# Kernel tuning notes

Measured on AMD Instinct MI355X. Metric: run time of the kernel, lower is better.

The kernel has to match this reference:

```python
import jax, jax.numpy as jnp
import numpy as np


def _ward_agglomerative(xf: np.ndarray, k: int) -> np.ndarray:
    """Ward-linkage agglomerative clustering (sklearn default), returning
    integer labels in [0, k) for each of the n rows of xf.

    Sequential Lance-Williams merge loop: this IS the algorithm's math and is
    inherently sequential (the reason this module has kernel headroom).
    Per-merge updates are fully vectorized over the n 'other' clusters.
    """
    xf = np.asarray(xf, dtype=np.float64)
    n = xf.shape[0]
    # initial squared-euclidean distances (Ward criterion on singletons)
    sq = np.sum(xf * xf, axis=1)
    d2 = sq[:, None] + sq[None, :] - 2.0 * (xf @ xf.T)
    np.maximum(d2, 0.0, out=d2)
    np.fill_diagonal(d2, np.inf)

    sizes = np.ones(n, dtype=np.float64)
    active = np.ones(n, dtype=bool)
    cluster_of = np.arange(n)  # point -> current representative cluster id
    idxs = np.arange(n)

    for _ in range(n - k):
        flat = np.argmin(d2)  # inactive rows/cols are +inf
        i, j = divmod(flat, n)
        if i > j:
            i, j = j, i
        dij = d2[i, j]
        si, sj = sizes[i], sizes[j]
        m = active.copy()
        m[i] = False
        m[j] = False
        sm = sizes[m]
        # Lance-Williams Ward update on squared distances (vectorized over m)
        new_d = ((si + sm) * d2[i, m] + (sj + sm) * d2[j, m] - sm * dij) / (si + sj + sm)
        d2[i, m] = new_d
        d2[m, i] = new_d
        sizes[i] = si + sj
        active[j] = False
        d2[j, :] = np.inf
        d2[:, j] = np.inf
        d2[i, i] = np.inf
        cluster_of[cluster_of == j] = i

    # relabel surviving cluster ids to 0..k-1 by first occurrence
    _, labels = np.unique(cluster_of, return_inverse=True)
    return labels.astype(np.int32)


def setup_inputs() -> dict:
    key = jax.random.key(0)
    x = jax.random.uniform(key, (4, 512, 96), dtype=jnp.float32)  # [B, N, D]
    return {"x": x, "num_clusters": 100}


def reference(x, num_clusters):
    # Faithful translation of HierarchicalClustering.forward:
    # flatten batch+tokens, Ward agglomerative clustering, one-hot scatter.
    B, N, D = x.shape
    xf = np.asarray(jax.device_get(x)).reshape(B * N, D)
    labels = _ward_agglomerative(xf, int(num_clusters))  # [B*N]
    onehot = jax.nn.one_hot(jnp.asarray(labels), int(num_clusters), dtype=jnp.float32)
    return onehot.reshape(B, N, int(num_clusters))
```

## Files before the change

kernel.cpp:

```cpp
#include <hip/hip_runtime.h>
#include <math.h>

#define NPTS   2048
#define DIM    96
#define PITCH  2048
#define TB     8
#define ROUNDS 48

__device__ double g_cent[DIM * PITCH];
__device__ double g_sz[NPTS];
__device__ double g_nrm[NPTS];
__device__ int    g_act[NPTS];
__device__ int    g_cidx[NPTS];
__device__ double g_nnv[NPTS];
__device__ int    g_nni[NPTS];
__device__ int    g_reci[NPTS];
__device__ int    g_recj[NPTS];
__device__ double g_rech[NPTS];
__device__ int    g_a, g_done, g_mcount;

__global__ void init_kernel(const float* __restrict__ x) {
    int p = blockIdx.x * 256 + threadIdx.x;
    if (p < NPTS) {
        double nr = 0.0;
        for (int d = 0; d < DIM; ++d) {
            double v = (double)x[p * DIM + d];
            g_cent[d * PITCH + p] = v;
            nr += v * v;
        }
        g_nrm[p] = nr; g_sz[p] = 1.0; g_act[p] = 1; g_cidx[p] = p;
        g_nni[p] = -1; g_nnv[p] = (double)INFINITY;
        g_reci[p] = 0; g_recj[p] = 0; g_rech[p] = (double)INFINITY;
    }
    if (p == 0) { g_a = NPTS; g_done = 0; g_mcount = 0; }
}

__global__ void __launch_bounds__(512) nn_pass() {
    if (g_done) return;
    const int a = g_a;
    const int tile0 = blockIdx.x * TB;
    if (tile0 >= a) return;
    const int t = threadIdx.x;

    __shared__ int    sIdx[TB];
    __shared__ double sMu[DIM * TB];
    __shared__ double sNb[TB], sSb[TB];
    __shared__ double sRedV[8 * TB];
    __shared__ int    sRedI[8 * TB];

    if (t < TB) {
        int cm   = tile0 + t;
        int orig = (cm < a) ? g_cidx[cm] : -1;
        sIdx[t] = orig;
        sNb[t]  = (orig >= 0) ? g_nrm[orig] : 0.0;
        sSb[t]  = (orig >= 0) ? g_sz[orig]  : 1.0;
    }
    __syncthreads();
    for (int e = t; e < DIM * TB; e += 512) {
        int col = sIdx[e & 7];
        sMu[e] = (col >= 0) ? g_cent[(e >> 3) * PITCH + col] : 0.0;
    }
    __syncthreads();

    int om[4]; bool vld[4];
#pragma unroll
    for (int q = 0; q < 4; ++q) {
        int m  = t + q * 512;
        vld[q] = (m < a);
        om[q]  = g_cidx[vld[q] ? m : (a - 1)];
    }

    double acc[4][TB];
#pragma unroll
    for (int q = 0; q < 4; ++q)
#pragma unroll
        for (int bi = 0; bi < TB; ++bi) acc[q][bi] = 0.0;

    for (int d = 0; d < DIM; ++d) {
        double mu[TB];
#pragma unroll
        for (int bi = 0; bi < TB; ++bi) mu[bi] = sMu[d * TB + bi];
        double x0 = g_cent[d * PITCH + om[0]];
        double x1 = g_cent[d * PITCH + om[1]];
        double x2 = g_cent[d * PITCH + om[2]];
        double x3 = g_cent[d * PITCH + om[3]];
#pragma unroll
        for (int bi = 0; bi < TB; ++bi) {
            acc[0][bi] += mu[bi] * x0;
            acc[1][bi] += mu[bi] * x1;
            acc[2][bi] += mu[bi] * x2;
            acc[3][bi] += mu[bi] * x3;
        }
    }

    double bv[TB]; int bidx[TB];
#pragma unroll
    for (int bi = 0; bi < TB; ++bi) { bv[bi] = (double)INFINITY; bidx[bi] = 0x7FFFFFFF; }
#pragma unroll
    for (int q = 0; q < 4; ++q) {
        if (!vld[q]) continue;
        int    cm = t + q * 512;
        double sm = g_sz[om[q]], nm = g_nrm[om[q]];
#pragma unroll
        for (int bi = 0; bi < TB; ++bi) {
            double f = (sSb[bi] * sm) / (sSb[bi] + sm);
            double D = (2.0 * f) * ((sNb[bi] + nm) - 2.0 * acc[q][bi]);
            if (cm != tile0 + bi && D < bv[bi]) { bv[bi] = D; bidx[bi] = om[q]; }
        }
    }

    const int lane = t & 63, w = t >> 6;
#pragma unroll
    for (int bi = 0; bi < TB; ++bi) {
        double v = bv[bi]; int ix = bidx[bi];
        for (int off = 1; off < 64; off <<= 1) {
            double ov = __shfl_xor(v, off);
            int    oi = __shfl_xor(ix, off);
            if (ov < v || (ov == v && oi < ix)) { v = ov; ix = oi; }
        }
        if (lane == 0) { sRedV[w * TB + bi] = v; sRedI[w * TB + bi] = ix; }
    }
    __syncthreads();
    if (t < TB && tile0 + t < a) {
        double v = sRedV[t]; int ix = sRedI[t];
        for (int w2 = 1; w2 < 8; ++w2) {
            double ov = sRedV[w2 * TB + t]; int oi = sRedI[w2 * TB + t];
            if (ov < v || (ov == v && oi < ix)) { v = ov; ix = oi; }
        }
        g_nnv[sIdx[t]] = v;
        g_nni[sIdx[t]] = ix;
    }
}

__global__ void __launch_bounds__(1024) merge_pass() {
    if (g_done) return;
    __shared__ int sWave[16];
    const int t = threadIdx.x, lane = t & 63, w = t >> 6;

    for (int b = t; b < NPTS; b += 1024) {
        int j = g_nni[b];
        if (j > b && j < NPTS && g_nni[j] == b) {
            int r = atomicAdd(&g_mcount, 1);
            g_reci[r] = b; g_recj[r] = j; g_rech[r] = g_nnv[b];
            double sb = g_sz[b], sj = g_sz[j], s2 = sb + sj;
            double nr = 0.0;
            for (int d = 0; d < DIM; ++d) {
                double v = (sb * g_cent[d * PITCH + b] + sj * g_cent[d * PITCH + j]) / s2;
                g_cent[d * PITCH + b] = v;
                nr += v * v;
            }
            g_sz[b] = s2; g_nrm[b] = nr;
            g_act[j] = 0; g_nni[j] = -1; g_nnv[j] = (double)INFINITY;
        }
    }
    __syncthreads();

    int e0 = 2 * t, e1 = 2 * t + 1;
    int c0 = g_act[e0], c1 = g_act[e1];
    int sum = c0 + c1;
    int v = sum;
    for (int off = 1; off < 64; off <<= 1) {
        int o = __shfl_up(v, off);
        if (lane >= off) v += o;
    }
    if (lane == 63) sWave[w] = v;
    __syncthreads();
    if (t == 0) {
        int run = 0;
        for (int i = 0; i < 16; ++i) { int x = sWave[i]; sWave[i] = run; run += x; }
    }
    __syncthreads();
    int base = sWave[w] + (v - sum);
    if (c0) g_cidx[base]      = e0;
    if (c1) g_cidx[base + c0] = e1;
    if (t == 1023) {
        int a2 = base + sum;
        g_a = a2;
        g_done = (a2 <= 1) ? 1 : 0;
    }
}

__global__ void __launch_bounds__(1024) finisher(const int* __restrict__ kptr,
                                                 float* __restrict__ out) {
    __shared__ double D0[NPTS];
    __shared__ int    I0[NPTS];
    __shared__ int    I1[NPTS];
    __shared__ int    I2[NPTS];
    __shared__ int    I3[NPTS];
    __shared__ int    I4[NPTS];
    __shared__ int    sNp;

    const int t = threadIdx.x, lane = t & 63, w = t >> 6;
    const int k = *kptr;
    int a = g_a;

    for (int guard = 0; guard < NPTS && a > 1; ++guard) {
        for (int b = w; b < NPTS; b += 16) {
            if (!g_act[b]) { if (lane == 0) { D0[b] = (double)INFINITY; I0[b] = -1; } continue; }
            double sb = g_sz[b], nb = g_nrm[b];
            double bvv = (double)INFINITY; int bii = 0x7FFFFFFF;
            for (int m = lane; m < NPTS; m += 64) {
                if (!g_act[m] || m == b) continue;
                double dot = 0.0;
                for (int d = 0; d < DIM; ++d)
                    dot += g_cent[d * PITCH + b] * g_cent[d * PITCH + m];
                double sm = g_sz[m], nm = g_nrm[m];
                double f = (sb * sm) / (sb + sm);
                double D = (2.0 * f) * ((nb + nm) - 2.0 * dot);
                if (D < bvv || (D == bvv && m < bii)) { bvv = D; bii = m; }
            }
            for (int off = 1; off < 64; off <<= 1) {
                double ov = __shfl_xor(bvv, off);
                int    oi = __shfl_xor(bii, off);
                if (ov < bvv || (ov == bvv && oi < bii)) { bvv = ov; bii = oi; }
            }
            if (lane == 0) { D0[b] = bvv; I0[b] = bii; }
        }
        __syncthreads();
        if (t == 0) sNp = 0;
        __syncthreads();
        for (int b = t; b < NPTS; b += 1024) {
            int j = I0[b];
            if (j > b && j < NPTS && I0[j] == b) {
                int r = atomicAdd(&g_mcount, 1);
                g_reci[r] = b; g_recj[r] = j; g_rech[r] = D0[b];
                double sb = g_sz[b], sj = g_sz[j], s2 = sb + sj;
                double nr = 0.0;
                for (int d = 0; d < DIM; ++d) {
                    double v = (sb * g_cent[d * PITCH + b] + sj * g_cent[d * PITCH + j]) / s2;
                    g_cent[d * PITCH + b] = v; nr += v * v;
                }
                g_sz[b] = s2; g_nrm[b] = nr; g_act[j] = 0;
                atomicAdd(&sNp, 1);
            }
        }
        __syncthreads();
        a -= sNp;
        __syncthreads();
    }

    const int M    = g_mcount;
    const int nsel = NPTS - k;
    __syncthreads();
    for (int e = t; e < NPTS; e += 1024) {
        D0[e] = (e < M) ? g_rech[e] : (double)INFINITY;
        I0[e] = e;
    }
    __syncthreads();
    for (int k2 = 2; k2 <= NPTS; k2 <<= 1) {
        for (int j2 = k2 >> 1; j2 > 0; j2 >>= 1) {
            for (int i = t; i < NPTS; i += 1024) {
                int ixj = i ^ j2;
                if (ixj > i) {
                    bool up = ((i & k2) == 0);
                    double a0 = D0[i], a1 = D0[ixj];
                    if (up ? (a0 > a1) : (a0 < a1)) {
                        D0[i] = a1; D0[ixj] = a0;
                        int ti_ = I0[i]; I0[i] = I0[ixj]; I0[ixj] = ti_;
                    }
                }
            }
            __syncthreads();
        }
    }
    for (int p = t; p < NPTS; p += 1024) I1[p] = p;
    __syncthreads();
    for (int r = t; r < nsel; r += 1024) {
        int rec = I0[r];
        I1[g_recj[rec]] = g_reci[rec];
    }
    __syncthreads();
    int* psrc = I1; int* pdst = I2;
    for (int it2 = 0; it2 < 11; ++it2) {
        for (int p = t; p < NPTS; p += 1024) pdst[p] = psrc[psrc[p]];
        __syncthreads();
        int* tp = psrc; psrc = pdst; pdst = tp;
    }
    for (int p = t; p < NPTS; p += 1024) I3[p] = (psrc[p] == p) ? 1 : 0;
    __syncthreads();
    int* rsrc = I3; int* rdst = I4;
    for (int off = 1; off < NPTS; off <<= 1) {
        for (int p = t; p < NPTS; p += 1024)
            rdst[p] = rsrc[p] + ((p >= off) ? rsrc[p - off] : 0);
        __syncthreads();
        int* tp = rsrc; rsrc = rdst; rdst = tp;
    }
    for (int p = t; p < NPTS; p += 1024) {
        int lbl = rsrc[psrc[p]] - 1;
        out[(size_t)p * k + lbl] = 1.0f;
    }
}

extern "C" void kernel_launch(void* const* d_in, const int* in_sizes, int n_in,
                              void* d_out, int out_size, void* d_ws, size_t ws_size,
                              hipStream_t stream) {
    const float* x    = (const float*)d_in[0];
    const int*   kptr = (const int*)d_in[1];
    float*       out  = (float*)d_out;

    hipMemsetAsync(d_out, 0, (size_t)out_size * sizeof(float), stream);
    init_kernel<<<8, 256, 0, stream>>>(x);
    for (int r = 0; r < ROUNDS; ++r) {
        nn_pass<<<NPTS / TB, 512, 0, stream>>>();
        merge_pass<<<1, 1024, 0, stream>>>();
    }
    finisher<<<1, 1024, 0, stream>>>(kptr, out);
}
```

Before: 3.475 ms.

## Fuse all clustering rounds into one persistent kernel with grid barriers

Replaces the fixed 48 rounds of nn_pass/merge_pass launches plus the separate init, memset and finisher with a single persistent kernel of 192 blocks. The blocks synchronise through an atomic grid barrier and each keeps its own copy of the active-cluster compaction in shared memory. Rounds run adaptively until fewer than 192 clusters remain, and block 0 then finishes alone. Merges are spread across waves, with 64 lanes working on the dimensions in parallel. This removes launch overhead and the wasted fixed rounds and the serial per-thread merge. The risks are grid-barrier deadlock if not all blocks are co-resident, plus high shared-memory use per block that may limit residency.

```diff
diff --git a/kernel.cpp b/kernel.cpp
--- a/kernel.cpp
+++ b/kernel.cpp
@@ -1,291 +1,336 @@
 #include <hip/hip_runtime.h>
 #include <math.h>
 
-#define NPTS   2048
-#define DIM    96
-#define PITCH  2048
-#define TB     8
-#define ROUNDS 48
+#define NPTS  2048
+#define DIM   96
+#define PITCH 2048
+#define TB    8
+#define NBLK  192
+#define NTHR  512
+#define TAIL  192
 
 __device__ double g_cent[DIM * PITCH];
 __device__ double g_sz[NPTS];
 __device__ double g_nrm[NPTS];
 __device__ int    g_act[NPTS];
-__device__ int    g_cidx[NPTS];
 __device__ double g_nnv[NPTS];
 __device__ int    g_nni[NPTS];
 __device__ int    g_reci[NPTS];
 __device__ int    g_recj[NPTS];
 __device__ double g_rech[NPTS];
-__device__ int    g_a, g_done, g_mcount;
-
-__global__ void init_kernel(const float* __restrict__ x) {
-    int p = blockIdx.x * 256 + threadIdx.x;
-    if (p < NPTS) {
+__device__ int    g_mcount;
+__device__ int    g_barcnt = 0;
+__device__ int    g_bargen = 0;
+
+__device__ __forceinline__ void gridbar() {
+    __syncthreads();
+    if (threadIdx.x == 0) {
+        __threadfence();
+        int gen = __hip_atomic_load(&g_bargen, __ATOMIC_RELAXED, __HIP_MEMORY_SCOPE_AGENT);
+        int prev = __hip_atomic_fetch_add(&g_barcnt, 1, __ATOMIC_ACQ_REL, __HIP_MEMORY_SCOPE_AGENT);
+        if (prev == NBLK - 1) {
+            __hip_atomic_store(&g_barcnt, 0, __ATOMIC_RELAXED, __HIP_MEMORY_SCOPE_AGENT);
+            __hip_atomic_store(&g_bargen, gen + 1, __ATOMIC_RELEASE, __HIP_MEMORY_SCOPE_AGENT);
+        } else {
+            while (__hip_atomic_load(&g_bargen, __ATOMIC_ACQUIRE, __HIP_MEMORY_SCOPE_AGENT) == gen)
+                __builtin_amdgcn_s_sleep(2);
+        }
+        __threadfence();
+    }
+    __syncthreads();
+}
+
+__device__ __forceinline__ int block_compact(unsigned short* sCidx, int* sWS) {
+    const int t = threadIdx.x, lane = t & 63, w = t >> 6;
+    int base = t * 4;
+    int c0 = g_act[base], c1 = g_act[base + 1], c2 = g_act[base + 2], c3 = g_act[base + 3];
+    int sum = c0 + c1 + c2 + c3;
+    int v = sum;
+#pragma unroll
+    for (int off = 1; off < 64; off <<= 1) {
+        int o = __shfl_up(v, off);
+        if (lane >= off) v += o;
+    }
+    if (lane == 63) sWS[w] = v;
+    __syncthreads();
+    if (t == 0) {
+        int run = 0;
+#pragma unroll
+        for (int i = 0; i < 8; ++i) { int x = sWS[i]; sWS[i] = run; run += x; }
+        sWS[8] = run;
+    }
+    __syncthreads();
+    int ex = sWS[w] + (v - sum);
+    if (c0) sCidx[ex] = (unsigned short)base;       ex += c0;
+    if (c1) sCidx[ex] = (unsigned short)(base + 1); ex += c1;
+    if (c2) sCidx[ex] = (unsigned short)(base + 2); ex += c2;
+    if (c3) sCidx[ex] = (unsigned short)(base + 3); ex += c3;
+    int a = sWS[8];
+    __syncthreads();
+    return a;
+}
+
+__device__ __forceinline__ void wave_merge(int b, int j, double hgt, int lane) {
+    double sb = g_sz[b], sj = g_sz[j], s2 = sb + sj;
+    int d0 = lane;
+    double v0 = (sb * g_cent[d0 * PITCH + b] + sj * g_cent[d0 * PITCH + j]) / s2;
+    g_cent[d0 * PITCH + b] = v0;
+    double v1 = 0.0;
+    if (lane < DIM - 64) {
+        int d1 = lane + 64;
+        v1 = (sb * g_cent[d1 * PITCH + b] + sj * g_cent[d1 * PITCH + j]) / s2;
+        g_cent[d1 * PITCH + b] = v1;
+    }
+    double pnr = v0 * v0 + v1 * v1;
+#pragma unroll
+    for (int off = 1; off < 64; off <<= 1)
+        pnr += __shfl_xor(pnr, off);
+    if (lane == 0) {
+        g_sz[b] = s2; g_nrm[b] = pnr; g_act[j] = 0;
+        int r = atomicAdd(&g_mcount, 1);
+        g_reci[r] = b; g_recj[r] = j; g_rech[r] = hgt;
+    }
+}
+
+__global__ void __launch_bounds__(NTHR) fused(const float* __restrict__ x,
+                                              const int* __restrict__ kptr,
+                                              float* __restrict__ out, int out_size) {
+    __shared__ unsigned short sCidx[NPTS];
+    __shared__ double sMu[TB * DIM];
+    __shared__ double sNb[TB], sSb[TB];
+    __shared__ int    sIdx[TB];
+    __shared__ double sRedV[64];
+    __shared__ int    sRedI[64];
+    __shared__ int    sPair[128];
+    __shared__ int    sNp;
+    __shared__ int    sWS[16];
+    __shared__ double fD0[NPTS];
+    __shared__ int    fI0[NPTS];
+    __shared__ int    fI1[NPTS];
+    __shared__ int    fI2[NPTS];
+    __shared__ int    fI3[NPTS];
+    __shared__ int    fI4[NPTS];
+
+    const int bid = blockIdx.x, t = threadIdx.x, lane = t & 63, w = t >> 6;
+
+    for (int i = bid * NTHR + t; i < out_size; i += NBLK * NTHR) out[i] = 0.0f;
+    for (int p = bid * NTHR + t; p < NPTS; p += NBLK * NTHR) {
         double nr = 0.0;
         for (int d = 0; d < DIM; ++d) {
             double v = (double)x[p * DIM + d];
             g_cent[d * PITCH + p] = v;
             nr += v * v;
         }
-        g_nrm[p] = nr; g_sz[p] = 1.0; g_act[p] = 1; g_cidx[p] = p;
-        g_nni[p] = -1; g_nnv[p] = (double)INFINITY;
-        g_reci[p] = 0; g_recj[p] = 0; g_rech[p] = (double)INFINITY;
-    }
-    if (p == 0) { g_a = NPTS; g_done = 0; g_mcount = 0; }
-}
-
-__global__ void __launch_bounds__(512) nn_pass() {
-    if (g_done) return;
-    const int a = g_a;
-    const int tile0 = blockIdx.x * TB;
-    if (tile0 >= a) return;
-    const int t = threadIdx.x;
-
-    __shared__ int    sIdx[TB];
-    __shared__ double sMu[DIM * TB];
-    __shared__ double sNb[TB], sSb[TB];
-    __shared__ double sRedV[8 * TB];
-    __shared__ int    sRedI[8 * TB];
-
-    if (t < TB) {
-        int cm   = tile0 + t;
-        int orig = (cm < a) ? g_cidx[cm] : -1;
-        sIdx[t] = orig;
-        sNb[t]  = (orig >= 0) ? g_nrm[orig] : 0.0;
-        sSb[t]  = (orig >= 0) ? g_sz[orig]  : 1.0;
-    }
-    __syncthreads();
-    for (int e = t; e < DIM * TB; e += 512) {
-        int col = sIdx[e & 7];
-        sMu[e] = (col >= 0) ? g_cent[(e >> 3) * PITCH + col] : 0.0;
-    }
-    __syncthreads();
-
-    int om[4]; bool vld[4];
-#pragma unroll
-    for (int q = 0; q < 4; ++q) {
-        int m  = t + q * 512;
-        vld[q] = (m < a);
-        om[q]  = g_cidx[vld[q] ? m : (a - 1)];
-    }
-
-    double acc[4][TB];
-#pragma unroll
-    for (int q = 0; q < 4; ++q)
-#pragma unroll
-        for (int bi = 0; bi < TB; ++bi) acc[q][bi] = 0.0;
-
-    for (int d = 0; d < DIM; ++d) {
-        double mu[TB];
-#pragma unroll
-        for (int bi = 0; bi < TB; ++bi) mu[bi] = sMu[d * TB + bi];
-        double x0 = g_cent[d * PITCH + om[0]];
-        double x1 = g_cent[d * PITCH + om[1]];
-        double x2 = g_cent[d * PITCH + om[2]];
-        double x3 = g_cent[d * PITCH + om[3]];
-#pragma unroll
-        for (int bi = 0; bi < TB; ++bi) {
-            acc[0][bi] += mu[bi] * x0;
-            acc[1][bi] += mu[bi] * x1;
-            acc[2][bi] += mu[bi] * x2;
-            acc[3][bi] += mu[bi] * x3;
-        }
-    }
-
-    double bv[TB]; int bidx[TB];
-#pragma unroll
-    for (int bi = 0; bi < TB; ++bi) { bv[bi] = (double)INFINITY; bidx[bi] = 0x7FFFFFFF; }
-#pragma unroll
-    for (int q = 0; q < 4; ++q) {
-        if (!vld[q]) continue;
-        int    cm = t + q * 512;
-        double sm = g_sz[om[q]], nm = g_nrm[om[q]];
-#pragma unroll
-        for (int bi = 0; bi < TB; ++bi) {
-            double f = (sSb[bi] * sm) / (sSb[bi] + sm);
-            double D = (2.0 * f) * ((sNb[bi] + nm) - 2.0 * acc[q][bi]);
-            if (cm != tile0 + bi && D < bv[bi]) { bv[bi] = D; bidx[bi] = om[q]; }
-        }
-    }
-
-    const int lane = t & 63, w = t >> 6;
-#pragma unroll
-    for (int bi = 0; bi < TB; ++bi) {
-        double v = bv[bi]; int ix = bidx[bi];
-        for (int off = 1; off < 64; off <<= 1) {
-            double ov = __shfl_xor(v, off);
-            int    oi = __shfl_xor(ix, off);
-            if (ov < v || (ov == v && oi < ix)) { v = ov; ix = oi; }
-        }
-        if (lane == 0) { sRedV[w * TB + bi] = v; sRedI[w * TB + bi] = ix; }
-    }
-    __syncthreads();
-    if (t < TB && tile0 + t < a) {
-        double v = sRedV[t]; int ix = sRedI[t];
-        for (int w2 = 1; w2 < 8; ++w2) {
-            double ov = sRedV[w2 * TB + t]; int oi = sRedI[w2 * TB + t];
-            if (ov < v || (ov == v && oi < ix)) { v = ov; ix = oi; }
-        }
-        g_nnv[sIdx[t]] = v;
-        g_nni[sIdx[t]] = ix;
-    }
-}
-
-__global__ void __launch_bounds__(1024) merge_pass() {
-    if (g_done) return;
-    __shared__ int sWave[16];
-    const int t = threadIdx.x, lane = t & 63, w = t >> 6;
-
-    for (int b = t; b < NPTS; b += 1024) {
-        int j = g_nni[b];
-        if (j > b && j < NPTS && g_nni[j] == b) {
-            int r = atomicAdd(&g_mcount, 1);
-            g_reci[r] = b; g_recj[r] = j; g_rech[r] = g_nnv[b];
-            double sb = g_sz[b], sj = g_sz[j], s2 = sb + sj;
-            double nr = 0.0;
+        g_nrm[p] = nr; g_sz[p] = 1.0; g_act[p] = 1;
+    }
+    if (bid == 0 && t == 0) g_mcount = 0;
+    gridbar();
+
+    int a = block_compact(sCidx, sWS);
+
+    while (a > TAIL) {
+        for (int tile0 = bid * TB; tile0 < a; tile0 += NBLK * TB) {
+            __syncthreads();
+            if (t < TB) {
+                int cm = tile0 + t;
+                int orig = (cm < a) ? (int)sCidx[cm] : -1;
+                sIdx[t] = orig;
+                sNb[t] = (orig >= 0) ? g_nrm[orig] : 0.0;
+                sSb[t] = (orig >= 0) ? g_sz[orig] : 1.0;
+            }
+            __syncthreads();
+            for (int e = t; e < DIM * TB; e += NTHR) {
+                int col = sIdx[e & 7];
+                sMu[e] = (col >= 0) ? g_cent[(e >> 3) * PITCH + col] : 0.0;
+            }
+            __syncthreads();
+
+            int om[4]; bool vld[4];
+#pragma unroll
+            for (int q = 0; q < 4; ++q) {
+                int m = t + q * NTHR;
+                vld[q] = (m < a);
+                om[q] = (int)sCidx[vld[q] ? m : (a - 1)];
+            }
+            double acc[4][TB];
+#pragma unroll
+            for (int q = 0; q < 4; ++q)
+#pragma unroll
+                for (int bi = 0; bi < TB; ++bi) acc[q][bi] = 0.0;
+
             for (int d = 0; d < DIM; ++d) {
-                double v = (sb * g_cent[d * PITCH + b] + sj * g_cent[d * PITCH + j]) / s2;
-                g_cent[d * PITCH + b] = v;
-                nr += v * v;
-            }
-            g_sz[b] = s2; g_nrm[b] = nr;
-            g_act[j] = 0; g_nni[j] = -1; g_nnv[j] = (double)INFINITY;
-        }
-    }
-    __syncthreads();
-
-    int e0 = 2 * t, e1 = 2 * t + 1;
-    int c0 = g_act[e0], c1 = g_act[e1];
-    int sum = c0 + c1;
-    int v = sum;
-    for (int off = 1; off < 64; off <<= 1) {
-        int o = __shfl_up(v, off);
-        if (lane >= off) v += o;
-    }
-    if (lane == 63) sWave[w] = v;
-    __syncthreads();
-    if (t == 0) {
-        int run = 0;
-        for (int i = 0; i < 16; ++i) { int x = sWave[i]; sWave[i] = run; run += x; }
-    }
-    __syncthreads();
-    int base = sWave[w] + (v - sum);
-    if (c0) g_cidx[base]      = e0;
-    if (c1) g_cidx[base + c0] = e1;
-    if (t == 1023) {
-        int a2 = base + sum;
-        g_a = a2;
-        g_done = (a2 <= 1) ? 1 : 0;
-    }
-}
-
-__global__ void __launch_bounds__(1024) finisher(const int* __restrict__ kptr,
-                                                 float* __restrict__ out) {
-    __shared__ double D0[NPTS];
-    __shared__ int    I0[NPTS];
-    __shared__ int    I1[NPTS];
-    __shared__ int    I2[NPTS];
-    __shared__ int    I3[NPTS];
-    __shared__ int    I4[NPTS];
-    __shared__ int    sNp;
-
-    const int t = threadIdx.x, lane = t & 63, w = t >> 6;
-    const int k = *kptr;
-    int a = g_a;
-
-    for (int guard = 0; guard < NPTS && a > 1; ++guard) {
-        for (int b = w; b < NPTS; b += 16) {
-            if (!g_act[b]) { if (lane == 0) { D0[b] = (double)INFINITY; I0[b] = -1; } continue; }
+                double mu[TB];
+#pragma unroll
+                for (int bi = 0; bi < TB; ++bi) mu[bi] = sMu[d * TB + bi];
+                double x0 = g_cent[d * PITCH + om[0]];
+                double x1 = g_cent[d * PITCH + om[1]];
+                double x2 = g_cent[d * PITCH + om[2]];
+                double x3 = g_cent[d * PITCH + om[3]];
+#pragma unroll
+                for (int bi = 0; bi < TB; ++bi) {
+                    acc[0][bi] += mu[bi] * x0;
+                    acc[1][bi] += mu[bi] * x1;
+                    acc[2][bi] += mu[bi] * x2;
+                    acc[3][bi] += mu[bi] * x3;
+                }
+            }
+
+            double bv[TB]; int bidx[TB];
+#pragma unroll
+            for (int bi = 0; bi < TB; ++bi) { bv[bi] = (double)INFINITY; bidx[bi] = 0x7FFFFFFF; }
+#pragma unroll
+            for (int q = 0; q < 4; ++q) {
+                if (!vld[q]) continue;
+                int cm = t + q * NTHR;
+                double sm = g_sz[om[q]], nm = g_nrm[om[q]];
+#pragma unroll
+                for (int bi = 0; bi < TB; ++bi) {
+                    double f = (sSb[bi] * sm) / (sSb[bi] + sm);
+                    double D = (2.0 * f) * ((sNb[bi] + nm) - 2.0 * acc[q][bi]);
+                    if (cm != tile0 + bi && D < bv[bi]) { bv[bi] = D; bidx[bi] = om[q]; }
+                }
+            }
+#pragma unroll
+            for (int bi = 0; bi < TB; ++bi) {
+                double v = bv[bi]; int ix = bidx[bi];
+                for (int off = 1; off < 64; off <<= 1) {
+                    double ov = __shfl_xor(v, off);
+                    int    oi = __shfl_xor(ix, off);
+                    if (ov < v || (ov == v && oi < ix)) { v = ov; ix = oi; }
+                }
+                if (lane == 0) { sRedV[w * TB + bi] = v; sRedI[w * TB + bi] = ix; }
+            }
+            __syncthreads();
+            if (t < TB && tile0 + t < a) {
+                double v = sRedV[t]; int ix = sRedI[t];
+                for (int w2 = 1; w2 < 8; ++w2) {
+                    double ov = sRedV[w2 * TB + t]; int oi = sRedI[w2 * TB + t];
+                    if (ov < v || (ov == v && oi < ix)) { v = ov; ix = oi; }
+                }
+                g_nnv[sIdx[t]] = v;
+                g_nni[sIdx[t]] = ix;
+            }
+        }
+        gridbar();
+
+        if (t == 0) sNp = 0;
+        __syncthreads();
+        for (int tile0 = bid * TB; tile0 < a; tile0 += NBLK * TB) {
+            int cm = tile0 + t;
+            if (t < TB && cm < a) {
+                int b = (int)sCidx[cm];
+                int j = g_nni[b];
+                if (j > b && g_nni[j] == b) {
+                    int s = atomicAdd(&sNp, 1);
+                    sPair[s] = (b << 16) | j;
+                }
+            }
+        }
+        __syncthreads();
+        int np = sNp;
+        for (int p = w; p < np; p += 8) {
+            int pk = sPair[p], b = pk >> 16, jj = pk & 0xFFFF;
+            wave_merge(b, jj, g_nnv[b], lane);
+        }
+        gridbar();
+        a = block_compact(sCidx, sWS);
+    }
+
+    if (bid != 0) return;
+
+    while (a > 1) {
+        for (int c = w; c < a; c += 8) {
+            int b = (int)sCidx[c];
             double sb = g_sz[b], nb = g_nrm[b];
-            double bvv = (double)INFINITY; int bii = 0x7FFFFFFF;
-            for (int m = lane; m < NPTS; m += 64) {
-                if (!g_act[m] || m == b) continue;
+            double bv = (double)INFINITY; int bi2 = 0x7FFFFFFF;
+            for (int cm = lane; cm < a; cm += 64) {
+                int m = (int)sCidx[cm];
+                if (m == b) continue;
                 double dot = 0.0;
                 for (int d = 0; d < DIM; ++d)
                     dot += g_cent[d * PITCH + b] * g_cent[d * PITCH + m];
                 double sm = g_sz[m], nm = g_nrm[m];
                 double f = (sb * sm) / (sb + sm);
                 double D = (2.0 * f) * ((nb + nm) - 2.0 * dot);
-                if (D < bvv || (D == bvv && m < bii)) { bvv = D; bii = m; }
-            }
+                if (D < bv || (D == bv && m < bi2)) { bv = D; bi2 = m; }
+            }
+#pragma unroll
             for (int off = 1; off < 64; off <<= 1) {
-                double ov = __shfl_xor(bvv, off);
-                int    oi = __shfl_xor(bii, off);
-                if (ov < bvv || (ov == bvv && oi < bii)) { bvv = ov; bii = oi; }
-            }
-            if (lane == 0) { D0[b] = bvv; I0[b] = bii; }
+                double ov = __shfl_xor(bv, off);
+                int    oi = __shfl_xor(bi2, off);
+                if (ov < bv || (ov == bv && oi < bi2)) { bv = ov; bi2 = oi; }
+            }
+            if (lane == 0) { fD0[b] = bv; fI0[b] = bi2; }
         }
         __syncthreads();
         if (t == 0) sNp = 0;
         __syncthreads();
-        for (int b = t; b < NPTS; b += 1024) {
-            int j = I0[b];
-            if (j > b && j < NPTS && I0[j] == b) {
-                int r = atomicAdd(&g_mcount, 1);
-                g_reci[r] = b; g_recj[r] = j; g_rech[r] = D0[b];
-                double sb = g_sz[b], sj = g_sz[j], s2 = sb + sj;
-                double nr = 0.0;
-                for (int d = 0; d < DIM; ++d) {
-                    double v = (sb * g_cent[d * PITCH + b] + sj * g_cent[d * PITCH + j]) / s2;
-                    g_cent[d * PITCH + b] = v; nr += v * v;
-                }
-                g_sz[b] = s2; g_nrm[b] = nr; g_act[j] = 0;
-                atomicAdd(&sNp, 1);
-            }
-        }
-        __syncthreads();
-        a -= sNp;
-        __syncthreads();
-    }
-
-    const int M    = g_mcount;
+        for (int c = t; c < a; c += NTHR) {
+            int b = (int)sCidx[c];
+            int j = fI0[b];
+            if (j > b && fI0[j] == b) {
+                int s = atomicAdd(&sNp, 1);
+                sPair[s] = (b << 16) | j;
+            }
+        }
+        __syncthreads();
+        int np = sNp;
+        for (int p = w; p < np; p += 8) {
+            int pk = sPair[p], b = pk >> 16, jj = pk & 0xFFFF;
+            wave_merge(b, jj, fD0[b], lane);
+        }
+        __syncthreads();
+        a = block_compact(sCidx, sWS);
+    }
+
+    const int k = *kptr;
+    const int M = g_mcount;
     const int nsel = NPTS - k;
     __syncthreads();
-    for (int e = t; e < NPTS; e += 1024) {
-        D0[e] = (e < M) ? g_rech[e] : (double)INFINITY;
-        I0[e] = e;
+    for (int e = t; e < NPTS; e += NTHR) {
+        fD0[e] = (e < M) ? g_rech[e] : (double)INFINITY;
+        fI0[e] = e;
     }
     __syncthreads();
     for (int k2 = 2; k2 <= NPTS; k2 <<= 1) {
         for (int j2 = k2 >> 1; j2 > 0; j2 >>= 1) {
-            for (int i = t; i < NPTS; i += 1024) {
+            for (int i = t; i < NPTS; i += NTHR) {
                 int ixj = i ^ j2;
                 if (ixj > i) {
                     bool up = ((i & k2) == 0);
-                    double a0 = D0[i], a1 = D0[ixj];
+                    double a0 = fD0[i], a1 = fD0[ixj];
                     if (up ? (a0 > a1) : (a0 < a1)) {
-                        D0[i] = a1; D0[ixj] = a0;
-                        int ti_ = I0[i]; I0[i] = I0[ixj]; I0[ixj] = ti_;
+                        fD0[i] = a1; fD0[ixj] = a0;
+                        int ti_ = fI0[i]; fI0[i] = fI0[ixj]; fI0[ixj] = ti_;
                     }
                 }
             }
             __syncthreads();
         }
     }
-    for (int p = t; p < NPTS; p += 1024) I1[p] = p;
-    __syncthreads();
-    for (int r = t; r < nsel; r += 1024) {
-        int rec = I0[r];
-        I1[g_recj[rec]] = g_reci[rec];
-    }
-    __syncthreads();
-    int* psrc = I1; int* pdst = I2;
+    for (int p = t; p < NPTS; p += NTHR) fI1[p] = p;
+    __syncthreads();
+    for (int r = t; r < nsel; r += NTHR) {
+        int rec = fI0[r];
+        fI1[g_recj[rec]] = g_reci[rec];
+    }
+    __syncthreads();
+    int* psrc = fI1; int* pdst = fI2;
     for (int it2 = 0; it2 < 11; ++it2) {
-        for (int p = t; p < NPTS; p += 1024) pdst[p] = psrc[psrc[p]];
+        for (int p = t; p < NPTS; p += NTHR) pdst[p] = psrc[psrc[p]];
         __syncthreads();
         int* tp = psrc; psrc = pdst; pdst = tp;
     }
-    for (int p = t; p < NPTS; p += 1024) I3[p] = (psrc[p] == p) ? 1 : 0;
-    __syncthreads();
-    int* rsrc = I3; int* rdst = I4;
+    for (int p = t; p < NPTS; p += NTHR) fI3[p] = (psrc[p] == p) ? 1 : 0;
+    __syncthreads();
+    int* rsrc = fI3; int* rdst = fI4;
     for (int off = 1; off < NPTS; off <<= 1) {
-        for (int p = t; p < NPTS; p += 1024)
+        for (int p = t; p < NPTS; p += NTHR)
             rdst[p] = rsrc[p] + ((p >= off) ? rsrc[p - off] : 0);
         __syncthreads();
         int* tp = rsrc; rsrc = rdst; rdst = tp;
     }
-    for (int p = t; p < NPTS; p += 1024) {
+    for (int p = t; p < NPTS; p += NTHR) {
         int lbl = rsrc[psrc[p]] - 1;
         out[(size_t)p * k + lbl] = 1.0f;
     }
@@ -298,11 +343,5 @@
     const int*   kptr = (const int*)d_in[1];
     float*       out  = (float*)d_out;
 
-    hipMemsetAsync(d_out, 0, (size_t)out_size * sizeof(float), stream);
-    init_kernel<<<8, 256, 0, stream>>>(x);
-    for (int r = 0; r < ROUNDS; ++r) {
-        nn_pass<<<NPTS / TB, 512, 0, stream>>>();
-        merge_pass<<<1, 1024, 0, stream>>>();
-    }
-    finisher<<<1, 1024, 0, stream>>>(kptr, out);
-}
+    fused<<<NBLK, NTHR, 0, stream>>>(x, kptr, out, out_size);
+}
```

Result: slower. 7.967 ms (+129.3%).
